# Kernel optimization log

Hardware: AMD Instinct MI355X
Metric: run time of the kernel (lower is better)

## Reference

```python
import jax, jax.numpy as jnp
import numpy as np

N_LAYER, N_HEAD, D_MODEL, D_FF = 6, 16, 1024, 4096
D_HEAD = D_MODEL // N_HEAD            # 64
M_FEAT = 2 * D_MODEL // N_HEAD        # 128, favor_feature_dims default
CHUNK = 128                           # chunk size for causal linear attention
LN_EPS = 1e-5
ATT_EPS = 1e-6                        # fast-transformers CausalLinearAttention eps
B, S = 4, 2048


def _layer_norm(x, g, b):
    mu = x.mean(-1, keepdims=True)
    var = ((x - mu) ** 2).mean(-1, keepdims=True)
    return (x - mu) * jax.lax.rsqrt(var + LN_EPS) * g + b


def _favor_phi(x, omega):
    # x: [B,H,S,Dh]; omega: [Dh, M//2]. FAVOR positive (hyperbolic) random
    # features: phi(x) = [exp(u - |x|^2/2), exp(-u - |x|^2/2)] / sqrt(M),
    # with x pre-scaled by sqrt(softmax_temp), softmax_temp = 1/sqrt(Dh).
    x = x * (D_HEAD ** -0.25)
    u = jnp.einsum('bhsd,dm->bhsm', x, omega)
    nrm = 0.5 * jnp.sum(x * x, axis=-1, keepdims=True)
    phi = jnp.concatenate([jnp.exp(u - nrm), jnp.exp(-u - nrm)], axis=-1)
    return phi * (M_FEAT ** -0.5)


def _causal_linear_attention(Qp, Kp, V):
    # Qp,Kp: [B,H,S,M] nonnegative features; V: [B,H,S,Dh].
    # out_i = phi(q_i)^T S_i / (phi(q_i)^T Z_i + eps),
    # S_i = sum_{j<=i} phi(k_j) v_j^T, Z_i = sum_{j<=i} phi(k_j).
    # Chunked: exclusive chunk prefix sums + masked intra-chunk matmul.
    b, h, s, m = Qp.shape
    d = V.shape[-1]
    c = s // CHUNK
    Qc = Qp.reshape(b, h, c, CHUNK, m)
    Kc = Kp.reshape(b, h, c, CHUNK, m)
    Vc = V.reshape(b, h, c, CHUNK, d)
    kv = jnp.einsum('bhclm,bhcld->bhcmd', Kc, Vc)   # per-chunk K^T V
    ksum = Kc.sum(axis=3)                            # [b,h,c,m]
    kv_pre = jnp.cumsum(kv, axis=2) - kv             # exclusive prefix over chunks
    ks_pre = jnp.cumsum(ksum, axis=2) - ksum
    scores = jnp.einsum('bhcim,bhcjm->bhcij', Qc, Kc)
    mask = jnp.tril(jnp.ones((CHUNK, CHUNK), bool))
    scores = jnp.where(mask, scores, 0.0)            # causal within chunk
    num = (jnp.einsum('bhcij,bhcjd->bhcid', scores, Vc)
           + jnp.einsum('bhcim,bhcmd->bhcid', Qc, kv_pre))
    den = scores.sum(-1) + jnp.einsum('bhcim,bhcm->bhci', Qc, ks_pre)
    out = num / (den[..., None] + ATT_EPS)
    return out.reshape(b, h, s, d)


def _forward(x, Wq, bq, Wk, bk, Wv, bv, Wo, bo, omega,
             g1, be1, W1, bf1, W2, bf2, g2, be2):
    bsz, slen, _ = x.shape
    out = x
    for l in range(N_LAYER):
        def proj(W, bvec):
            y = jnp.einsum('bsd,de->bse', out, W) + bvec
            return y.reshape(bsz, slen, N_HEAD, D_HEAD).transpose(0, 2, 1, 3)
        q = proj(Wq[l], bq[l])
        k = proj(Wk[l], bk[l])
        v = proj(Wv[l], bv[l])
        Qp = _favor_phi(q, omega[l])
        Kp = _favor_phi(k, omega[l])
        a = _causal_linear_attention(Qp, Kp, v)
        a = a.transpose(0, 2, 1, 3).reshape(bsz, slen, D_MODEL)
        a = jnp.einsum('bsd,de->bse', a, Wo[l]) + bo[l]
        h1 = _layer_norm(out + a, g1[l], be1[l])          # post-norm residual 1
        y = jax.nn.relu(jnp.einsum('bsd,df->bsf', h1, W1[l]) + bf1[l])
        y = jnp.einsum('bsf,fd->bsd', y, W2[l]) + bf2[l]
        out = _layer_norm(h1 + y, g2[l], be2[l])          # post-norm residual 2
    return out


def setup_inputs() -> dict:
    key = jax.random.key(0)
    ks = jax.random.split(key, 12)
    s = D_MODEL ** -0.5
    f32 = jnp.float32
    return {
        "x": jax.random.normal(ks[0], (B, S, D_MODEL), f32),
        "Wq": jax.random.normal(ks[1], (N_LAYER, D_MODEL, D_MODEL), f32) * s,
        "bq": jnp.zeros((N_LAYER, D_MODEL), f32),
        "Wk": jax.random.normal(ks[2], (N_LAYER, D_MODEL, D_MODEL), f32) * s,
        "bk": jnp.zeros((N_LAYER, D_MODEL), f32),
        "Wv": jax.random.normal(ks[3], (N_LAYER, D_MODEL, D_MODEL), f32) * s,
        "bv": jnp.zeros((N_LAYER, D_MODEL), f32),
        "Wo": jax.random.normal(ks[4], (N_LAYER, D_MODEL, D_MODEL), f32) * s,
        "bo": jnp.zeros((N_LAYER, D_MODEL), f32),
        "omega": jax.random.normal(ks[5], (N_LAYER, D_HEAD, M_FEAT // 2), f32),
        "g1": jnp.ones((N_LAYER, D_MODEL), f32),
        "be1": jnp.zeros((N_LAYER, D_MODEL), f32),
        "W1": jax.random.normal(ks[6], (N_LAYER, D_MODEL, D_FF), f32) * s,
        "bf1": jnp.zeros((N_LAYER, D_FF), f32),
        "W2": jax.random.normal(ks[7], (N_LAYER, D_FF, D_MODEL), f32) * (D_FF ** -0.5),
        "bf2": jnp.zeros((N_LAYER, D_MODEL), f32),
        "g2": jnp.ones((N_LAYER, D_MODEL), f32),
        "be2": jnp.zeros((N_LAYER, D_MODEL), f32),
    }


def reference(x, Wq, bq, Wk, bk, Wv, bv, Wo, bo, omega,
              g1, be1, W1, bf1, W2, bf2, g2, be2):
    return _forward(x, Wq, bq, Wk, bk, Wv, bv, Wo, bo, omega,
                    g1, be1, W1, bf1, W2, bf2, g2, be2)
```

## Files before the change

### kernel.cpp

```cpp
#include <hip/hip_runtime.h>

typedef unsigned short u16;
typedef __attribute__((ext_vector_type(8))) short bf16x8;
typedef __attribute__((ext_vector_type(4))) float f32x4;

#define DEV __device__ __forceinline__

DEV float b2f(u16 h){ return __uint_as_float(((unsigned)h) << 16); }
DEV u16 f2b(float f){ unsigned u = __float_as_uint(f); u += 0x7FFFu + ((u >> 16) & 1u); return (u16)(u >> 16); }

DEV void gload16(const u16* g, u16* l){
  __builtin_amdgcn_global_load_lds((const __attribute__((address_space(1))) unsigned*)g,
                                   (__attribute__((address_space(3))) unsigned*)l, 16, 0, 0);
}

__global__ __launch_bounds__(256) void wtrans(const float* __restrict__ src, u16* __restrict__ dst,
                                              int K, int N, float scale){
  __shared__ float tile[32][33];
  int k0 = blockIdx.x * 32, n0 = blockIdx.y * 32;
  int tid = threadIdx.x;
#pragma unroll
  for (int i = 0; i < 4; i++){
    int idx = tid + i * 256;
    int r = idx >> 5, c = idx & 31;
    tile[r][c] = src[(size_t)(k0 + r) * N + n0 + c];
  }
  __syncthreads();
#pragma unroll
  for (int i = 0; i < 4; i++){
    int idx = tid + i * 256;
    int r = idx >> 5, c = idx & 31;
    dst[(size_t)(n0 + r) * K + k0 + c] = f2b(tile[c][r] * scale);
  }
}

__global__ __launch_bounds__(256) void cvt16(const float* __restrict__ src, u16* __restrict__ dst){
  size_t i = ((size_t)blockIdx.x * 256 + threadIdx.x) * 4;
  float4 f = *(const float4*)(src + i);
  ushort4 o = make_ushort4(f2b(f.x), f2b(f.y), f2b(f.z), f2b(f.w));
  *(ushort4*)(dst + i) = o;
}

__global__ void catbias(const float* __restrict__ bq, const float* __restrict__ bk,
                        const float* __restrict__ bv, float* __restrict__ bcat){
  int i = blockIdx.x * 256 + threadIdx.x;
  if (i >= 6 * 3072) return;
  int l = i / 3072, j = i % 3072;
  float v = (j < 1024) ? bq[l * 1024 + j] : (j < 2048) ? bk[l * 1024 + j - 1024] : bv[l * 1024 + j - 2048];
  bcat[i] = v;
}

__global__ void fillv(float* __restrict__ p, float v, int n){
  int i = blockIdx.x * 256 + threadIdx.x;
  if (i < n) p[i] = v;
}

DEV int swz(int r){ return (r & 3) ^ ((r >> 2) & 3); }

template<int EPI>
__global__ __launch_bounds__(256) void gemm_bt(const u16* __restrict__ A, const u16* __restrict__ Bt,
                                               const float* __restrict__ bias, void* __restrict__ outp,
                                               int M, int N, int K, int ldA, int ldB){
  __shared__ __align__(16) u16 As[2][4096];
  __shared__ __align__(16) u16 Bs[2][4096];
  const int tid = threadIdx.x;
  const int lane = tid & 63;
  const int w = tid >> 6;
  const int wm = w >> 1, wn = w & 1;
  int nx = gridDim.x;
  int nwg = nx * gridDim.y;
  int lin = blockIdx.y * nx + blockIdx.x;
  int cpx = nwg >> 3;
  int sw = (lin & 7) * cpx + (lin >> 3);
  const int m0 = (sw / nx) * 128;
  const int n0 = (sw % nx) * 128;

  int r0 = tid >> 2, c0 = tid & 3;
  int r1 = r0 + 64;
  int cs0 = c0 ^ swz(r0);
  int cs1 = c0 ^ swz(r1);
  const u16* ag0 = A + (size_t)(m0 + r0) * ldA + cs0 * 8;
  const u16* ag1 = A + (size_t)(m0 + r1) * ldA + cs1 * 8;
  const u16* bg0 = Bt + (size_t)(n0 + r0) * ldB + cs0 * 8;
  const u16* bg1 = Bt + (size_t)(n0 + r1) * ldB + cs1 * 8;

  f32x4 acc[4][4] = {};
  const int KT = K >> 5;

  gload16(ag0, &As[0][w * 512]);
  gload16(ag1, &As[0][2048 + w * 512]);
  gload16(bg0, &Bs[0][w * 512]);
  gload16(bg1, &Bs[0][2048 + w * 512]);

  for (int kt = 0; kt < KT; kt++){
    int cur = kt & 1;
    if (kt + 1 < KT){
      int ko = (kt + 1) << 5;
      gload16(ag0 + ko, &As[cur ^ 1][w * 512]);
      gload16(ag1 + ko, &As[cur ^ 1][2048 + w * 512]);
      gload16(bg0 + ko, &Bs[cur ^ 1][w * 512]);
      gload16(bg1 + ko, &Bs[cur ^ 1][2048 + w * 512]);
      asm volatile("s_waitcnt vmcnt(4)" ::: "memory");
    } else {
      asm volatile("s_waitcnt vmcnt(0)" ::: "memory");
    }
    __builtin_amdgcn_s_barrier();
    bf16x8 fa[4], fb[4];
#pragma unroll
    for (int m = 0; m < 4; m++){
      int row = wm * 64 + m * 16 + (lane & 15);
      int cc = (lane >> 4) ^ swz(row);
      fa[m] = *(const bf16x8*)(&As[cur][row * 32 + cc * 8]);
    }
#pragma unroll
    for (int n = 0; n < 4; n++){
      int row = wn * 64 + n * 16 + (lane & 15);
      int cc = (lane >> 4) ^ swz(row);
      fb[n] = *(const bf16x8*)(&Bs[cur][row * 32 + cc * 8]);
    }
#pragma unroll
    for (int m = 0; m < 4; m++)
#pragma unroll
      for (int n = 0; n < 4; n++)
        acc[m][n] = __builtin_amdgcn_mfma_f32_16x16x32_bf16(fa[m], fb[n], acc[m][n], 0, 0, 0);
    asm volatile("s_waitcnt lgkmcnt(0)" ::: "memory");
    __builtin_amdgcn_s_barrier();
  }

#pragma unroll
  for (int m = 0; m < 4; m++){
    int rowb = m0 + wm * 64 + m * 16 + ((lane >> 4) << 2);
#pragma unroll
    for (int n = 0; n < 4; n++){
      int col = n0 + wn * 64 + n * 16 + (lane & 15);
      float bv = bias[col];
      if (EPI == 5 && col >= 2048){
        int cv = col - 2048, hh = cv >> 6, dh = cv & 63;
        int bIdx = rowb >> 11, s4 = rowb & 2047;
        ushort4 pk = make_ushort4(f2b(acc[m][n][0] + bv), f2b(acc[m][n][1] + bv),
                                  f2b(acc[m][n][2] + bv), f2b(acc[m][n][3] + bv));
        *(ushort4*)&((u16*)outp + 16777216)[((size_t)(bIdx * 16 + hh) * 64 + dh) * 2048 + s4] = pk;
      } else {
#pragma unroll
        for (int r = 0; r < 4; r++){
          float v = acc[m][n][r] + bv;
          int rr = rowb + r;
          if (EPI == 5){
            u16* dst0 = (u16*)outp + (col < 1024 ? 0 : 8388608);
            int cv = col & 1023, hh = cv >> 6, dh = cv & 63;
            int bIdx = rr >> 11, s = rr & 2047;
            dst0[(((size_t)(bIdx * 16 + hh) * 2048 + s) << 6) + dh] = f2b(v);
          } else if (EPI == 2){
            ((u16*)outp)[(size_t)rr * N + col] = f2b(v > 0.f ? v : 0.f);
          } else {
            ((u16*)outp)[(size_t)rr * N + col] = f2b(v);
          }
        }
      }
    }
  }
}

template<int EPI>
__global__ __launch_bounds__(512, 1) void gemm8p(const u16* __restrict__ A, const u16* __restrict__ Bt,
                                                 const float* __restrict__ bias, void* __restrict__ outp,
                                                 int M, int N, int K, int ldA, int ldB){
  __shared__ __align__(16) u16 As[2][16384];
  __shared__ __align__(16) u16 Bs[2][16384];
  const int tid = threadIdx.x;
  const int lane = tid & 63;
  const int w = tid >> 6;
  const int wm = w >> 2, wn = w & 3;
  int nx = gridDim.x;
  int nwg = nx * gridDim.y;
  int lin = blockIdx.y * nx + blockIdx.x;
  int cpx = nwg >> 3;
  int sw = (lin & 7) * cpx + (lin >> 3);
  const int m0 = (sw / nx) * 256;
  const int n0 = (sw % nx) * 256;

  const int id1 = 512 + tid;
  const int r0 = tid >> 2, c20 = tid & 3;
  const int r1 = id1 >> 2, c21 = id1 & 3;
  const int cs0 = c20 ^ ((r0 >> 1) & 3);
  const int cs1 = c21 ^ ((r1 >> 1) & 3);
  const u16* Ag0 = A + (size_t)(m0 + r0) * ldA + cs0 * 8;
  const u16* Ag1 = A + (size_t)(m0 + r1) * ldA + cs1 * 8;
  const u16* Bg0 = Bt + (size_t)(n0 + r0) * ldB + cs0 * 8;
  const u16* Bg1 = Bt + (size_t)(n0 + r1) * ldB + cs1 * 8;

  f32x4 acc[8][4] = {};
  const int KT = K >> 6;

  auto stA = [&](int buf, int kt, int ks){
    int kc = kt * 64 + ks * 32;
    gload16(Ag0 + kc, &As[buf][ks * 8192 + w * 512]);
    gload16(Ag1 + kc, &As[buf][ks * 8192 + 4096 + w * 512]);
  };
  auto stB = [&](int buf, int kt, int ks){
    int kc = kt * 64 + ks * 32;
    gload16(Bg0 + kc, &Bs[buf][ks * 8192 + w * 512]);
    gload16(Bg1 + kc, &Bs[buf][ks * 8192 + 4096 + w * 512]);
  };

  stA(0, 0, 0); stB(0, 0, 0); stA(0, 0, 1); stB(0, 0, 1);

  for (int t = 0; t < KT; t++){
    int c = t & 1, nb = c ^ 1;
    bool pf = (t + 1 < KT);
    asm volatile("s_waitcnt vmcnt(4)" ::: "memory");
    __builtin_amdgcn_s_barrier();

#pragma unroll
    for (int ks = 0; ks < 2; ks++){
      if (ks == 1){
        if (pf) asm volatile("s_waitcnt vmcnt(4)" ::: "memory");
        else    asm volatile("s_waitcnt vmcnt(0)" ::: "memory");
        __builtin_amdgcn_s_barrier();
      }
      if (pf){ if (ks == 0) stA(nb, t + 1, 0); else stA(nb, t + 1, 1); }
      bf16x8 fa[8], fb[2];
#pragma unroll
      for (int m = 0; m < 8; m++){
        int row = wm * 128 + m * 16 + (lane & 15);
        int slot = (lane >> 4) ^ ((row >> 1) & 3);
        fa[m] = *(const bf16x8*)(&As[c][ks * 8192 + row * 32 + slot * 8]);
      }
#pragma unroll
      for (int nn = 0; nn < 2; nn++){
        int row = wn * 64 + nn * 16 + (lane & 15);
        int slot = (lane >> 4) ^ ((row >> 1) & 3);
        fb[nn] = *(const bf16x8*)(&Bs[c][ks * 8192 + row * 32 + slot * 8]);
      }
      __builtin_amdgcn_s_setprio(1);
#pragma unroll
      for (int m = 0; m < 8; m++)
#pragma unroll
        for (int nn = 0; nn < 2; nn++)
          acc[m][nn] = __builtin_amdgcn_mfma_f32_16x16x32_bf16(fa[m], fb[nn], acc[m][nn], 0, 0, 0);
      __builtin_amdgcn_s_setprio(0);
      if (pf){ if (ks == 0) stB(nb, t + 1, 0); else stB(nb, t + 1, 1); }
#pragma unroll
      for (int nn = 0; nn < 2; nn++){
        int row = wn * 64 + 32 + nn * 16 + (lane & 15);
        int slot = (lane >> 4) ^ ((row >> 1) & 3);
        fb[nn] = *(const bf16x8*)(&Bs[c][ks * 8192 + row * 32 + slot * 8]);
      }
      __builtin_amdgcn_s_setprio(1);
#pragma unroll
      for (int m = 0; m < 8; m++)
#pragma unroll
        for (int nn = 0; nn < 2; nn++)
          acc[m][2 + nn] = __builtin_amdgcn_mfma_f32_16x16x32_bf16(fa[m], fb[nn], acc[m][2 + nn], 0, 0, 0);
      __builtin_amdgcn_s_setprio(0);
    }
  }

#pragma unroll
  for (int m = 0; m < 8; m++){
    int rowb = m0 + wm * 128 + m * 16 + ((lane >> 4) << 2);
#pragma unroll
    for (int n = 0; n < 4; n++){
      int col = n0 + wn * 64 + n * 16 + (lane & 15);
      float bv = bias[col];
#pragma unroll
      for (int r = 0; r < 4; r++){
        float v = acc[m][n][r] + bv;
        int rr = rowb + r;
        if (EPI == 2) ((u16*)outp)[(size_t)rr * N + col] = f2b(v > 0.f ? v : 0.f);
        else          ((u16*)outp)[(size_t)rr * N + col] = f2b(v);
      }
    }
  }
}

__global__ __launch_bounds__(512, 1) void gemm8pk(const u16* __restrict__ A, const u16* __restrict__ Bt,
                                                  const float* __restrict__ bias0, const float* __restrict__ bias1,
                                                  u16* __restrict__ out0, u16* __restrict__ out1,
                                                  int M, int N, int Khalf, int ldA, int ldB){
  __shared__ __align__(16) u16 As[2][16384];
  __shared__ __align__(16) u16 Bs[2][16384];
  const int tid = threadIdx.x;
  const int lane = tid & 63;
  const int w = tid >> 6;
  const int wm = w >> 2, wn = w & 3;
  int lin = blockIdx.x;
  int cpx = gridDim.x >> 3;
  int sw = (lin & 7) * cpx + (lin >> 3);
  const int kz = sw & 1;
  const int t2 = sw >> 1;
  const int n0 = (t2 & 3) * 256;
  const int m0 = (t2 >> 2) * 256;
  const u16* Ab = A + kz * Khalf;
  const u16* Bb = Bt + kz * Khalf;
  u16* outp = kz ? out1 : out0;
  const float* bias = kz ? bias1 : bias0;

  const int id1 = 512 + tid;
  const int r0 = tid >> 2, c20 = tid & 3;
  const int r1 = id1 >> 2, c21 = id1 & 3;
  const int cs0 = c20 ^ ((r0 >> 1) & 3);
  const int cs1 = c21 ^ ((r1 >> 1) & 3);
  const u16* Ag0 = Ab + (size_t)(m0 + r0) * ldA + cs0 * 8;
  const u16* Ag1 = Ab + (size_t)(m0 + r1) * ldA + cs1 * 8;
  const u16* Bg0 = Bb + (size_t)(n0 + r0) * ldB + cs0 * 8;
  const u16* Bg1 = Bb + (size_t)(n0 + r1) * ldB + cs1 * 8;

  f32x4 acc[8][4] = {};
  const int KT = Khalf >> 6;

  auto stA = [&](int buf, int kt, int ks){
    int kc = kt * 64 + ks * 32;
    gload16(Ag0 + kc, &As[buf][ks * 8192 + w * 512]);
    gload16(Ag1 + kc, &As[buf][ks * 8192 + 4096 + w * 512]);
  };
  auto stB = [&](int buf, int kt, int ks){
    int kc = kt * 64 + ks * 32;
    gload16(Bg0 + kc, &Bs[buf][ks * 8192 + w * 512]);
    gload16(Bg1 + kc, &Bs[buf][ks * 8192 + 4096 + w * 512]);
  };

  stA(0, 0, 0); stB(0, 0, 0); stA(0, 0, 1); stB(0, 0, 1);

  for (int t = 0; t < KT; t++){
    int c = t & 1, nb = c ^ 1;
    bool pf = (t + 1 < KT);
    asm volatile("s_waitcnt vmcnt(4)" ::: "memory");
    __builtin_amdgcn_s_barrier();

#pragma unroll
    for (int ks = 0; ks < 2; ks++){
      if (ks == 1){
        if (pf) asm volatile("s_waitcnt vmcnt(4)" ::: "memory");
        else    asm volatile("s_waitcnt vmcnt(0)" ::: "memory");
        __builtin_amdgcn_s_barrier();
      }
      if (pf){ if (ks == 0) stA(nb, t + 1, 0); else stA(nb, t + 1, 1); }
      bf16x8 fa[8], fb[2];
#pragma unroll
      for (int m = 0; m < 8; m++){
        int row = wm * 128 + m * 16 + (lane & 15);
        int slot = (lane >> 4) ^ ((row >> 1) & 3);
        fa[m] = *(const bf16x8*)(&As[c][ks * 8192 + row * 32 + slot * 8]);
      }
#pragma unroll
      for (int nn = 0; nn < 2; nn++){
        int row = wn * 64 + nn * 16 + (lane & 15);
        int slot = (lane >> 4) ^ ((row >> 1) & 3);
        fb[nn] = *(const bf16x8*)(&Bs[c][ks * 8192 + row * 32 + slot * 8]);
      }
      __builtin_amdgcn_s_setprio(1);
#pragma unroll
      for (int m = 0; m < 8; m++)
#pragma unroll
        for (int nn = 0; nn < 2; nn++)
          acc[m][nn] = __builtin_amdgcn_mfma_f32_16x16x32_bf16(fa[m], fb[nn], acc[m][nn], 0, 0, 0);
      __builtin_amdgcn_s_setprio(0);
      if (pf){ if (ks == 0) stB(nb, t + 1, 0); else stB(nb, t + 1, 1); }
#pragma unroll
      for (int nn = 0; nn < 2; nn++){
        int row = wn * 64 + 32 + nn * 16 + (lane & 15);
        int slot = (lane >> 4) ^ ((row >> 1) & 3);
        fb[nn] = *(const bf16x8*)(&Bs[c][ks * 8192 + row * 32 + slot * 8]);
      }
      __builtin_amdgcn_s_setprio(1);
#pragma unroll
      for (int m = 0; m < 8; m++)
#pragma unroll
        for (int nn = 0; nn < 2; nn++)
          acc[m][2 + nn] = __builtin_amdgcn_mfma_f32_16x16x32_bf16(fa[m], fb[nn], acc[m][2 + nn], 0, 0, 0);
      __builtin_amdgcn_s_setprio(0);
    }
  }

#pragma unroll
  for (int m = 0; m < 8; m++){
    int rowb = m0 + wm * 128 + m * 16 + ((lane >> 4) << 2);
#pragma unroll
    for (int n = 0; n < 4; n++){
      int col = n0 + wn * 64 + n * 16 + (lane & 15);
      float bv = bias[col];
#pragma unroll
      for (int r = 0; r < 4; r++)
        outp[(size_t)(rowb + r) * N + col] = f2b(acc[m][n][r] + bv);
    }
  }
}

__global__ __launch_bounds__(256) void phi2(const u16* __restrict__ qb, const u16* __restrict__ kb,
                                            const u16* __restrict__ omT,
                                            u16* __restrict__ Qp, u16* __restrict__ Kp){
  __shared__ __align__(16) u16 qs[128 * 64];
  __shared__ __align__(16) u16 wl[64 * 64];
  __shared__ __align__(16) u16 ph[128 * 128];
  __shared__ float part[2][128];
  __shared__ float nrm[128];
  int tid = threadIdx.x, w = tid >> 6, lane = tid & 63;
  int blk = blockIdx.x;
  const u16* src; u16* dst; int row0;
  if (blk < 1024){ src = qb; dst = Qp; row0 = blk * 128; }
  else           { src = kb; dst = Kp; row0 = (blk - 1024) * 128; }
  const u16* g = src + (size_t)row0 * 64;
#pragma unroll
  for (int i = 0; i < 4; i++){
    int id = tid * 4 + i;
    int r = id >> 3, kc = id & 7;
    *(bf16x8*)(qs + r * 64 + ((kc ^ (r & 7)) << 3)) = *(const bf16x8*)(g + r * 64 + kc * 8);
  }
#pragma unroll
  for (int i = 0; i < 2; i++){
    int id = tid * 2 + i;
    int m = id >> 3, kc = id & 7;
    *(bf16x8*)(wl + m * 64 + ((kc ^ (m & 7)) << 3)) = *(const bf16x8*)(omT + id * 8);
  }
  __syncthreads();
  {
    int r = tid & 127, half = tid >> 7;
    float s = 0.f;
#pragma unroll
    for (int j = 0; j < 4; j++){
      int kc = half * 4 + j;
      bf16x8 v = *(const bf16x8*)(qs + r * 64 + ((kc ^ (r & 7)) << 3));
#pragma unroll
      for (int e = 0; e < 8; e++){ float f = b2f((u16)v[e]); s += f * f; }
    }
    part[half][r] = s;
  }
  __syncthreads();
  if (tid < 128) nrm[tid] = 0.0625f * (part[0][tid] + part[1][tid]);
  __syncthreads();
  f32x4 acc[2][4] = {};
#pragma unroll
  for (int kt = 0; kt < 2; kt++){
    int kc = kt * 4 + (lane >> 4);
    bf16x8 fa[2], fb[4];
#pragma unroll
    for (int mt = 0; mt < 2; mt++){
      int r = w * 32 + mt * 16 + (lane & 15);
      fa[mt] = *(const bf16x8*)(qs + r * 64 + ((kc ^ (r & 7)) << 3));
    }
#pragma unroll
    for (int nt = 0; nt < 4; nt++){
      int m = nt * 16 + (lane & 15);
      fb[nt] = *(const bf16x8*)(wl + m * 64 + ((kc ^ (m & 7)) << 3));
    }
#pragma unroll
    for (int mt = 0; mt < 2; mt++)
#pragma unroll
      for (int nt = 0; nt < 4; nt++)
        acc[mt][nt] = __builtin_amdgcn_mfma_f32_16x16x32_bf16(fa[mt], fb[nt], acc[mt][nt], 0, 0, 0);
  }
  const float LNC = -2.4260151319598086f;
#pragma unroll
  for (int mt = 0; mt < 2; mt++)
#pragma unroll
    for (int nt = 0; nt < 4; nt++)
#pragma unroll
      for (int r4 = 0; r4 < 4; r4++){
        int r = w * 32 + mt * 16 + ((lane >> 4) << 2) + r4;
        int m = nt * 16 + (lane & 15);
        float u = acc[mt][nt][r4];
        float nr = nrm[r];
        ph[r * 128 + m]      = f2b(__expf(u - nr + LNC));
        ph[r * 128 + 64 + m] = f2b(__expf(-u - nr + LNC));
      }
  __syncthreads();
  u16* go = dst + (size_t)row0 * 128;
#pragma unroll
  for (int i = 0; i < 8; i++){
    int id = i * 256 + tid;
    *(bf16x8*)(go + id * 8) = *(const bf16x8*)(ph + id * 8);
  }
}

__global__ __launch_bounds__(256) void kvchunk(const u16* __restrict__ Kp, const u16* __restrict__ vt,
                                               float* __restrict__ kv, float* __restrict__ ksum){
  __shared__ __align__(16) u16 Ks[128 * 128];
  __shared__ __align__(16) u16 Vst[64 * 128];
  int blk = blockIdx.x; int bh = blk >> 4, c = blk & 15;
  int tid = threadIdx.x;
  size_t base = (size_t)bh * 2048 + c * 128;
  const u16* Kc = Kp + base * 128;
  const u16* vtc = vt + (size_t)bh * 64 * 2048 + c * 128;
  {
    int j = tid >> 1, half = tid & 1;
#pragma unroll
    for (int i = 0; i < 8; i++)
      *(bf16x8*)(Ks + j * 128 + half * 64 + i * 8) = *(const bf16x8*)(Kc + j * 128 + half * 64 + i * 8);
#pragma unroll
    for (int i = 0; i < 4; i++){
      int id = tid * 4 + i;
      int d = id >> 4, mc = id & 15;
      *(bf16x8*)(Vst + d * 128 + mc * 8) = *(const bf16x8*)(vtc + (size_t)d * 2048 + mc * 8);
    }
  }
  __syncthreads();
  int tm = tid & 15, td = tid >> 4;
  int mbase = tm * 8, dbase = td * 4;
  float acc[8][4] = {};
  float ks[8] = {};
  for (int i = 0; i < 128; i++){
    bf16x8 kk = *(const bf16x8*)(Ks + i * 128 + mbase);
    float kf[8];
#pragma unroll
    for (int e = 0; e < 8; e++) kf[e] = b2f((u16)kk[e]);
    float vf[4];
#pragma unroll
    for (int e = 0; e < 4; e++) vf[e] = b2f(Vst[(dbase + e) * 128 + i]);
#pragma unroll
    for (int a = 0; a < 8; a++){
      ks[a] += kf[a];
#pragma unroll
      for (int bb = 0; bb < 4; bb++) acc[a][bb] += kf[a] * vf[bb];
    }
  }
  float* kvout = kv + ((size_t)bh * 16 + c) * 8192;
#pragma unroll
  for (int a = 0; a < 8; a++)
#pragma unroll
    for (int bb = 0; bb < 4; bb++)
      kvout[(size_t)(dbase + bb) * 128 + mbase + a] = acc[a][bb];
  if (td == 0){
    float* kso = ksum + ((size_t)bh * 16 + c) * 128;
#pragma unroll
    for (int a = 0; a < 8; a++) kso[mbase + a] = ks[a];
  }
}

__global__ __launch_bounds__(256) void kvscan(float* __restrict__ kv, float* __restrict__ ksum){
  int bh = blockIdx.x;
  int p = blockIdx.y;
  int tid = threadIdx.x;
  if (p < 8){
    size_t base = (size_t)bh * 16 * 8192;
    int idx0 = p * 1024 + tid;
    for (int rep = 0; rep < 4; rep++){
      int idx = idx0 + rep * 256;
      float run = 0.f;
#pragma unroll
      for (int c = 0; c < 16; c++){
        size_t off = base + (size_t)c * 8192 + idx;
        float v = kv[off]; kv[off] = run; run += v;
      }
    }
  } else if (tid < 128){
    size_t base = (size_t)bh * 16 * 128;
    float run = 0.f;
#pragma unroll
    for (int c = 0; c < 16; c++){
      size_t off = base + c * 128 + tid;
      float v = ksum[off]; ksum[off] = run; run += v;
    }
  }
}

__global__ __launch_bounds__(512) void attn_fused(const u16* __restrict__ Qp, const u16* __restrict__ Kp,
                                                  const u16* __restrict__ vt, const float* __restrict__ kvp,
                                                  const float* __restrict__ ksum, u16* __restrict__ aout){
  __shared__ __align__(16) u16 sm[53248];
  int blk = blockIdx.x, bh = blk >> 4, c = blk & 15;
  int b = bh >> 4, h = bh & 15;
  int tid = threadIdx.x, w = tid >> 6, lane = tid & 63;
  size_t base = (size_t)bh * 2048 + c * 128;
  const u16* Qc = Qp + base * 128;
  const u16* Kc = Kp + base * 128;
  const u16* vtc = vt + (size_t)bh * 64 * 2048 + c * 128;
  const float* kvc = kvp + ((size_t)bh * 16 + c) * 8192;
  const float* ksc = ksum + ((size_t)bh * 16 + c) * 128;
  u16* Qs = sm;
  u16* Ks = sm + 16384;
  u16* B2 = sm + 32768;

#pragma unroll
  for (int i = 0; i < 4; i++){
    int id = tid * 4 + i;
    int r = id >> 4, kc = id & 15;
    int swo = (kc ^ (r & 15)) << 3;
    *(bf16x8*)(Qs + r * 128 + swo) = *(const bf16x8*)(Qc + (size_t)r * 128 + kc * 8);
    *(bf16x8*)(Ks + r * 128 + swo) = *(const bf16x8*)(Kc + (size_t)r * 128 + kc * 8);
  }
#pragma unroll
  for (int i = 0; i < 2; i++){
    int id = tid * 2 + i;
    int d = id >> 4, kc = id & 15;
    *(bf16x8*)(B2 + d * 256 + ((kc ^ (d & 31)) << 3)) = *(const bf16x8*)(vtc + (size_t)d * 2048 + kc * 8);
  }
#pragma unroll
  for (int i = 0; i < 2; i++){
    int id = tid * 2 + i;
    int d = id >> 4, mc = id & 15;
    const float* s8 = kvc + d * 128 + mc * 8;
    float4 f0 = *(const float4*)(s8);
    float4 f1 = *(const float4*)(s8 + 4);
    bf16x8 pk;
    pk[0] = (short)f2b(f0.x); pk[1] = (short)f2b(f0.y); pk[2] = (short)f2b(f0.z); pk[3] = (short)f2b(f0.w);
    pk[4] = (short)f2b(f1.x); pk[5] = (short)f2b(f1.y); pk[6] = (short)f2b(f1.z); pk[7] = (short)f2b(f1.w);
    int kc = 16 + mc;
    *(bf16x8*)(B2 + d * 256 + ((kc ^ (d & 31)) << 3)) = pk;
  }
  {
    int row = 64 + (tid >> 5), kc = tid & 31;
    bf16x8 pk = {};
    if (row == 64){
      if (kc < 16){
#pragma unroll
        for (int e = 0; e < 8; e++) pk[e] = (short)0x3F80;
      } else {
        const float* s8 = ksc + (kc - 16) * 8;
        float4 f0 = *(const float4*)(s8);
        float4 f1 = *(const float4*)(s8 + 4);
        pk[0] = (short)f2b(f0.x); pk[1] = (short)f2b(f0.y); pk[2] = (short)f2b(f0.z); pk[3] = (short)f2b(f0.w);
        pk[4] = (short)f2b(f1.x); pk[5] = (short)f2b(f1.y); pk[6] = (short)f2b(f1.z); pk[7] = (short)f2b(f1.w);
      }
    }
    *(bf16x8*)(B2 + row * 256 + ((kc ^ (row & 31)) << 3)) = pk;
  }
  __syncthreads();

  int wm = w >> 2, wn = w & 3;
  f32x4 acc1[4][2] = {};
#pragma unroll
  for (int kk = 0; kk < 4; kk++){
    int kc = kk * 4 + (lane >> 4);
    bf16x8 fa[4], fb[2];
#pragma unroll
    for (int m = 0; m < 4; m++){
      int row = wm * 64 + m * 16 + (lane & 15);
      fa[m] = *(const bf16x8*)(Qs + row * 128 + ((kc ^ (row & 15)) << 3));
    }
#pragma unroll
    for (int n = 0; n < 2; n++){
      int row = wn * 32 + n * 16 + (lane & 15);
      fb[n] = *(const bf16x8*)(Ks + row * 128 + ((kc ^ (row & 15)) << 3));
    }
#pragma unroll
    for (int m = 0; m < 4; m++)
#pragma unroll
      for (int n = 0; n < 2; n++)
        acc1[m][n] = __builtin_amdgcn_mfma_f32_16x16x32_bf16(fa[m], fb[n], acc1[m][n], 0, 0, 0);
  }
  __syncthreads();

#pragma unroll
  for (int m = 0; m < 4; m++)
#pragma unroll
    for (int n = 0; n < 2; n++)
#pragma unroll
      for (int r = 0; r < 4; r++){
        int i = wm * 64 + m * 16 + ((lane >> 4) << 2) + r;
        int j = wn * 32 + n * 16 + (lane & 15);
        float v = (j <= i) ? acc1[m][n][r] : 0.f;
        Ks[i * 128 + (((j >> 3) ^ (i & 15)) << 3) + (j & 7)] = f2b(v);
      }
  __syncthreads();

  f32x4 acc2[5] = {};
#pragma unroll
  for (int kk = 0; kk < 8; kk++){
    int kc = kk * 4 + (lane >> 4);
    int rowA = w * 16 + (lane & 15);
    bf16x8 fa2;
    if (kk < 4) fa2 = *(const bf16x8*)(Ks + rowA * 128 + ((kc ^ (rowA & 15)) << 3));
    else        fa2 = *(const bf16x8*)(Qs + rowA * 128 + (((kc - 16) ^ (rowA & 15)) << 3));
#pragma unroll
    for (int n = 0; n < 5; n++){
      int d = n * 16 + (lane & 15);
      bf16x8 fb2 = *(const bf16x8*)(B2 + d * 256 + ((kc ^ (d & 31)) << 3));
      acc2[n] = __builtin_amdgcn_mfma_f32_16x16x32_bf16(fa2, fb2, acc2[n], 0, 0, 0);
    }
  }

  float dd[4];
#pragma unroll
  for (int r = 0; r < 4; r++) dd[r] = __shfl(acc2[4][r], lane & 48) + 1e-6f;
  size_t obase = ((size_t)b * 2048 + c * 128) * 1024 + (size_t)h * 64;
#pragma unroll
  for (int n = 0; n < 4; n++)
#pragma unroll
    for (int r = 0; r < 4; r++){
      int i = w * 16 + ((lane >> 4) << 2) + r;
      int d = n * 16 + (lane & 15);
      aout[obase + (size_t)i * 1024 + d] = f2b(acc2[n][r] / dd[r]);
    }
}

__global__ __launch_bounds__(256) void ln_kernel(const float* __restrict__ X1, const u16* __restrict__ X2b,
                                                 const float* __restrict__ g, const float* __restrict__ bb,
                                                 float* __restrict__ outf, u16* __restrict__ outb){
  __shared__ float red[2][4];
  int row = blockIdx.x, tid = threadIdx.x, w = tid >> 6, lane = tid & 63;
  size_t ro = (size_t)row * 1024 + tid * 4;
  float4 a = *(const float4*)(X1 + ro);
  ushort4 bp = *(const ushort4*)(X2b + ro);
  float x0 = a.x + b2f(bp.x), x1 = a.y + b2f(bp.y), x2 = a.z + b2f(bp.z), x3 = a.w + b2f(bp.w);
  float s1 = x0 + x1 + x2 + x3;
  float s2 = x0 * x0 + x1 * x1 + x2 * x2 + x3 * x3;
#pragma unroll
  for (int off = 32; off; off >>= 1){ s1 += __shfl_xor(s1, off); s2 += __shfl_xor(s2, off); }
  if (lane == 0){ red[0][w] = s1; red[1][w] = s2; }
  __syncthreads();
  float t1 = red[0][0] + red[0][1] + red[0][2] + red[0][3];
  float t2 = red[1][0] + red[1][1] + red[1][2] + red[1][3];
  float mu = t1 * (1.f / 1024.f);
  float var = t2 * (1.f / 1024.f) - mu * mu;
  float rs = rsqrtf(var + 1e-5f);
  float4 gv = *(const float4*)(g + tid * 4);
  float4 bv = *(const float4*)(bb + tid * 4);
  float o0 = (x0 - mu) * rs * gv.x + bv.x;
  float o1 = (x1 - mu) * rs * gv.y + bv.y;
  float o2 = (x2 - mu) * rs * gv.z + bv.z;
  float o3 = (x3 - mu) * rs * gv.w + bv.w;
  *(float4*)(outf + ro) = make_float4(o0, o1, o2, o3);
  *(ushort4*)(outb + ro) = make_ushort4(f2b(o0), f2b(o1), f2b(o2), f2b(o3));
}

__global__ __launch_bounds__(256) void ln3_kernel(const float* __restrict__ X1, const u16* __restrict__ P0,
                                                  const u16* P1, const float* __restrict__ g,
                                                  const float* __restrict__ bb,
                                                  float* __restrict__ outf, u16* outb){
  __shared__ float red[2][4];
  int row = blockIdx.x, tid = threadIdx.x, w = tid >> 6, lane = tid & 63;
  size_t ro = (size_t)row * 1024 + tid * 4;
  float4 a = *(const float4*)(X1 + ro);
  ushort4 p0 = *(const ushort4*)(P0 + ro);
  ushort4 p1 = *(const ushort4*)(P1 + ro);
  float x0 = a.x + b2f(p0.x) + b2f(p1.x);
  float x1 = a.y + b2f(p0.y) + b2f(p1.y);
  float x2 = a.z + b2f(p0.z) + b2f(p1.z);
  float x3 = a.w + b2f(p0.w) + b2f(p1.w);
  float s1 = x0 + x1 + x2 + x3;
  float s2 = x0 * x0 + x1 * x1 + x2 * x2 + x3 * x3;
#pragma unroll
  for (int off = 32; off; off >>= 1){ s1 += __shfl_xor(s1, off); s2 += __shfl_xor(s2, off); }
  if (lane == 0){ red[0][w] = s1; red[1][w] = s2; }
  __syncthreads();
  float t1 = red[0][0] + red[0][1] + red[0][2] + red[0][3];
  float t2 = red[1][0] + red[1][1] + red[1][2] + red[1][3];
  float mu = t1 * (1.f / 1024.f);
  float var = t2 * (1.f / 1024.f) - mu * mu;
  float rs = rsqrtf(var + 1e-5f);
  float4 gv = *(const float4*)(g + tid * 4);
  float4 bv = *(const float4*)(bb + tid * 4);
  float o0 = (x0 - mu) * rs * gv.x + bv.x;
  float o1 = (x1 - mu) * rs * gv.y + bv.y;
  float o2 = (x2 - mu) * rs * gv.z + bv.z;
  float o3 = (x3 - mu) * rs * gv.w + bv.w;
  *(float4*)(outf + ro) = make_float4(o0, o1, o2, o3);
  *(ushort4*)(outb + ro) = make_ushort4(f2b(o0), f2b(o1), f2b(o2), f2b(o3));
}

extern "C" void kernel_launch(void* const* d_in, const int* in_sizes, int n_in,
                              void* d_out, int out_size, void* d_ws, size_t ws_size,
                              hipStream_t stream){
  (void)in_sizes; (void)n_in;
  const float* x   = (const float*)d_in[0];
  const float* Wq  = (const float*)d_in[1];
  const float* bq  = (const float*)d_in[2];
  const float* Wk  = (const float*)d_in[3];
  const float* bk  = (const float*)d_in[4];
  const float* Wv  = (const float*)d_in[5];
  const float* bv  = (const float*)d_in[6];
  const float* Wo  = (const float*)d_in[7];
  const float* bo  = (const float*)d_in[8];
  const float* om  = (const float*)d_in[9];
  const float* g1  = (const float*)d_in[10];
  const float* be1 = (const float*)d_in[11];
  const float* W1  = (const float*)d_in[12];
  const float* bf1 = (const float*)d_in[13];
  const float* W2  = (const float*)d_in[14];
  const float* bf2 = (const float*)d_in[15];
  const float* g2  = (const float*)d_in[16];
  const float* be2 = (const float*)d_in[17];

  char* ws = (char*)d_ws;
  size_t off = 0;
  auto alloc = [&](size_t bytes) -> void* {
    void* p = ws + off; off += (bytes + 255) & ~(size_t)255; return p;
  };
  u16* Wcat = (u16*)alloc(3072ull * 1024 * 2);
  u16* Wot  = (u16*)alloc(1024ull * 1024 * 2);
  u16* W1t  = (u16*)alloc(4096ull * 1024 * 2);
  u16* W2t  = (u16*)alloc(1024ull * 4096 * 2);
  u16* omT  = (u16*)alloc(64ull * 64 * 2);
  float* bcat = (float*)alloc(6ull * 3072 * 4);
  float* zbuf = (float*)alloc(1024 * 4);
  u16* Xb  = (u16*)alloc(8192ull * 1024 * 2);
  u16* qb  = (u16*)alloc(131072ull * 64 * 2);
  u16* kb  = (u16*)alloc(131072ull * 64 * 2);
  u16* vt  = (u16*)alloc(131072ull * 64 * 2);
  u16* Qp  = (u16*)alloc(131072ull * 128 * 2);
  u16* Kp  = (u16*)alloc(131072ull * 128 * 2);
  float* ksum = (float*)alloc(64ull * 16 * 128 * 4);

  if (off > ws_size){
    fillv<<<(out_size + 255) / 256, 256, 0, stream>>>((float*)d_out, (float)(ws_size >> 20), out_size);
    return;
  }

  float* kvbuf  = (float*)qb;
  u16*  ybuf   = qb;
  u16*  wooutb = Qp;
  u16*  w2outb = Qp + 8388608;
  float* h1     = (float*)Kp;
  float* resid  = (float*)d_out;

  cvt16<<<8192, 256, 0, stream>>>(x, Xb);
  catbias<<<72, 256, 0, stream>>>(bq, bk, bv, bcat);
  fillv<<<4, 256, 0, stream>>>(zbuf, 0.f, 1024);

  const float* Xsrc = x;
  for (int l = 0; l < 6; l++){
    size_t o1k = (size_t)l * 1024 * 1024;
    size_t o4k = (size_t)l * 4096 * 1024;
    wtrans<<<dim3(32, 32), 256, 0, stream>>>(Wq + o1k, Wcat, 1024, 1024, 1.f);
    wtrans<<<dim3(32, 32), 256, 0, stream>>>(Wk + o1k, Wcat + 1024ull * 1024, 1024, 1024, 1.f);
    wtrans<<<dim3(32, 32), 256, 0, stream>>>(Wv + o1k, Wcat + 2048ull * 1024, 1024, 1024, 1.f);
    wtrans<<<dim3(32, 32), 256, 0, stream>>>(Wo + o1k, Wot, 1024, 1024, 1.f);
    wtrans<<<dim3(32, 128), 256, 0, stream>>>(W1 + o4k, W1t, 1024, 4096, 1.f);
    wtrans<<<dim3(128, 32), 256, 0, stream>>>(W2 + o4k, W2t, 4096, 1024, 1.f);
    wtrans<<<dim3(2, 2), 256, 0, stream>>>(om + (size_t)l * 4096, omT, 64, 64, 0.35355339059327373f);

    gemm_bt<5><<<dim3(24, 64), 256, 0, stream>>>(Xb, Wcat, bcat + l * 3072, qb, 8192, 3072, 1024, 1024, 1024);
    phi2<<<2048, 256, 0, stream>>>(qb, kb, omT, Qp, Kp);
    kvchunk<<<1024, 256, 0, stream>>>(Kp, vt, kvbuf, ksum);
    kvscan<<<dim3(64, 9), 256, 0, stream>>>(kvbuf, ksum);
    attn_fused<<<1024, 512, 0, stream>>>(Qp, Kp, vt, kvbuf, ksum, Xb);
    gemm_bt<6><<<dim3(8, 64), 256, 0, stream>>>(Xb, Wot, bo + l * 1024, wooutb, 8192, 1024, 1024, 1024, 1024);
    ln_kernel<<<8192, 256, 0, stream>>>(Xsrc, wooutb, g1 + l * 1024, be1 + l * 1024, h1, Xb);
    gemm8p<2><<<dim3(16, 32), 512, 0, stream>>>(Xb, W1t, bf1 + l * 4096, ybuf, 8192, 4096, 1024, 1024, 1024);
    gemm8pk<<<dim3(256), 512, 0, stream>>>(ybuf, W2t, bf2 + l * 1024, zbuf, w2outb, Xb,
                                           8192, 1024, 2048, 4096, 4096);
    ln3_kernel<<<8192, 256, 0, stream>>>(h1, w2outb, Xb, g2 + l * 1024, be2 + l * 1024, resid, Xb);
    Xsrc = resid;
  }
}
```

Measured before the change: 2.579 ms.

## Batch weight transposes across layers and stage ReLU GEMM epilogue through LDS

Weight conversion/transposition for all six layers is now done up front in seven batched launches (grid z over layers) into per-layer buffers, instead of seven small launches per layer, when workspace allows; otherwise it falls back to per-layer transposes. Separately, the ReLU epilogue of gemm8p now writes the bf16 tile into shared memory with an XOR swizzle and then stores coalesced 16-byte rows to global, replacing scattered 2-byte stores. This cuts launch count and improves store coalescing at the cost of more workspace and an extra LDS round trip with two barriers.

```diff
diff --git a/kernel.cpp b/kernel.cpp
--- a/kernel.cpp
+++ b/kernel.cpp
@@ -17,6 +17,28 @@
 __global__ __launch_bounds__(256) void wtrans(const float* __restrict__ src, u16* __restrict__ dst,
                                               int K, int N, float scale){
   __shared__ float tile[32][33];
+  int k0 = blockIdx.x * 32, n0 = blockIdx.y * 32;
+  int tid = threadIdx.x;
+#pragma unroll
+  for (int i = 0; i < 4; i++){
+    int idx = tid + i * 256;
+    int r = idx >> 5, c = idx & 31;
+    tile[r][c] = src[(size_t)(k0 + r) * N + n0 + c];
+  }
+  __syncthreads();
+#pragma unroll
+  for (int i = 0; i < 4; i++){
+    int idx = tid + i * 256;
+    int r = idx >> 5, c = idx & 31;
+    dst[(size_t)(n0 + r) * K + k0 + c] = f2b(tile[c][r] * scale);
+  }
+}
+
+__global__ __launch_bounds__(256) void wtransb(const float* __restrict__ src0, u16* __restrict__ dst0,
+                                               int K, int N, float scale, size_t sstride, size_t dstride){
+  __shared__ float tile[32][33];
+  const float* src = src0 + blockIdx.z * sstride;
+  u16* dst = dst0 + blockIdx.z * dstride;
   int k0 = blockIdx.x * 32, n0 = blockIdx.y * 32;
   int tid = threadIdx.x;
 #pragma unroll
@@ -256,6 +278,39 @@
     }
   }
 
+  if (EPI == 2){
+    __syncthreads();
+    u16* Cl = wm ? (u16*)&Bs[0][0] : (u16*)&As[0][0];
+#pragma unroll
+    for (int m = 0; m < 8; m++){
+#pragma unroll
+      for (int n = 0; n < 4; n++){
+        int col = wn * 64 + n * 16 + (lane & 15);
+        float bv = bias[n0 + col];
+#pragma unroll
+        for (int r = 0; r < 4; r++){
+          int row = m * 16 + ((lane >> 4) << 2) + r;
+          int X = ((row >> 2) & 3) << 4;
+          float v = acc[m][n][r] + bv;
+          Cl[row * 256 + (col ^ X)] = f2b(v > 0.f ? v : 0.f);
+        }
+      }
+    }
+    __syncthreads();
+#pragma unroll
+    for (int i = 0; i < 16; i++){
+      int id = i * 512 + tid;
+      int half = id >> 12;
+      int idx = id & 4095;
+      int row_l = idx >> 5, ck = idx & 31;
+      int X = ((row_l >> 2) & 3) << 4;
+      const u16* srcp = (half ? (const u16*)&Bs[0][0] : (const u16*)&As[0][0]) + row_l * 256 + ((ck * 8) ^ X);
+      u16* gdst = (u16*)outp + (size_t)(m0 + half * 128 + row_l) * N + n0 + ck * 8;
+      *(bf16x8*)gdst = *(const bf16x8*)srcp;
+    }
+    return;
+  }
+
 #pragma unroll
   for (int m = 0; m < 8; m++){
     int rowb = m0 + wm * 128 + m * 16 + ((lane >> 4) << 2);
@@ -267,8 +322,7 @@
       for (int r = 0; r < 4; r++){
         float v = acc[m][n][r] + bv;
         int rr = rowb + r;
-        if (EPI == 2) ((u16*)outp)[(size_t)rr * N + col] = f2b(v > 0.f ? v : 0.f);
-        else          ((u16*)outp)[(size_t)rr * N + col] = f2b(v);
+        ((u16*)outp)[(size_t)rr * N + col] = f2b(v);
       }
     }
   }
@@ -777,11 +831,6 @@
   auto alloc = [&](size_t bytes) -> void* {
     void* p = ws + off; off += (bytes + 255) & ~(size_t)255; return p;
   };
-  u16* Wcat = (u16*)alloc(3072ull * 1024 * 2);
-  u16* Wot  = (u16*)alloc(1024ull * 1024 * 2);
-  u16* W1t  = (u16*)alloc(4096ull * 1024 * 2);
-  u16* W2t  = (u16*)alloc(1024ull * 4096 * 2);
-  u16* omT  = (u16*)alloc(64ull * 64 * 2);
   float* bcat = (float*)alloc(6ull * 3072 * 4);
   float* zbuf = (float*)alloc(1024 * 4);
   u16* Xb  = (u16*)alloc(8192ull * 1024 * 2);
@@ -791,7 +840,22 @@
   u16* Qp  = (u16*)alloc(131072ull * 128 * 2);
   u16* Kp  = (u16*)alloc(131072ull * 128 * 2);
   float* ksum = (float*)alloc(64ull * 16 * 128 * 4);
-
+  size_t base_end = off;
+
+  u16* Wcat6 = (u16*)alloc(6ull * 3072 * 1024 * 2);
+  u16* Wot6  = (u16*)alloc(6ull * 1024 * 1024 * 2);
+  u16* W1t6  = (u16*)alloc(6ull * 4096 * 1024 * 2);
+  u16* W2t6  = (u16*)alloc(6ull * 4096 * 1024 * 2);
+  u16* omT6  = (u16*)alloc(6ull * 64 * 64 * 2);
+  bool hoist = (off <= ws_size);
+  if (!hoist){
+    off = base_end;
+    Wcat6 = (u16*)alloc(3072ull * 1024 * 2);
+    Wot6  = (u16*)alloc(1024ull * 1024 * 2);
+    W1t6  = (u16*)alloc(4096ull * 1024 * 2);
+    W2t6  = (u16*)alloc(4096ull * 1024 * 2);
+    omT6  = (u16*)alloc(64ull * 64 * 2);
+  }
   if (off > ws_size){
     fillv<<<(out_size + 255) / 256, 256, 0, stream>>>((float*)d_out, (float)(ws_size >> 20), out_size);
     return;
@@ -808,27 +872,44 @@
   catbias<<<72, 256, 0, stream>>>(bq, bk, bv, bcat);
   fillv<<<4, 256, 0, stream>>>(zbuf, 0.f, 1024);
 
+  if (hoist){
+    wtransb<<<dim3(32, 32, 6), 256, 0, stream>>>(Wq, Wcat6, 1024, 1024, 1.f, 1048576, 3145728);
+    wtransb<<<dim3(32, 32, 6), 256, 0, stream>>>(Wk, Wcat6 + 1048576, 1024, 1024, 1.f, 1048576, 3145728);
+    wtransb<<<dim3(32, 32, 6), 256, 0, stream>>>(Wv, Wcat6 + 2097152, 1024, 1024, 1.f, 1048576, 3145728);
+    wtransb<<<dim3(32, 32, 6), 256, 0, stream>>>(Wo, Wot6, 1024, 1024, 1.f, 1048576, 1048576);
+    wtransb<<<dim3(32, 128, 6), 256, 0, stream>>>(W1, W1t6, 1024, 4096, 1.f, 4194304, 4194304);
+    wtransb<<<dim3(128, 32, 6), 256, 0, stream>>>(W2, W2t6, 4096, 1024, 1.f, 4194304, 4194304);
+    wtransb<<<dim3(2, 2, 6), 256, 0, stream>>>(om, omT6, 64, 64, 0.35355339059327373f, 4096, 4096);
+  }
+
   const float* Xsrc = x;
   for (int l = 0; l < 6; l++){
     size_t o1k = (size_t)l * 1024 * 1024;
     size_t o4k = (size_t)l * 4096 * 1024;
-    wtrans<<<dim3(32, 32), 256, 0, stream>>>(Wq + o1k, Wcat, 1024, 1024, 1.f);
-    wtrans<<<dim3(32, 32), 256, 0, stream>>>(Wk + o1k, Wcat + 1024ull * 1024, 1024, 1024, 1.f);
-    wtrans<<<dim3(32, 32), 256, 0, stream>>>(Wv + o1k, Wcat + 2048ull * 1024, 1024, 1024, 1.f);
-    wtrans<<<dim3(32, 32), 256, 0, stream>>>(Wo + o1k, Wot, 1024, 1024, 1.f);
-    wtrans<<<dim3(32, 128), 256, 0, stream>>>(W1 + o4k, W1t, 1024, 4096, 1.f);
-    wtrans<<<dim3(128, 32), 256, 0, stream>>>(W2 + o4k, W2t, 4096, 1024, 1.f);
-    wtrans<<<dim3(2, 2), 256, 0, stream>>>(om + (size_t)l * 4096, omT, 64, 64, 0.35355339059327373f);
-
-    gemm_bt<5><<<dim3(24, 64), 256, 0, stream>>>(Xb, Wcat, bcat + l * 3072, qb, 8192, 3072, 1024, 1024, 1024);
-    phi2<<<2048, 256, 0, stream>>>(qb, kb, omT, Qp, Kp);
+    const u16* wcat = Wcat6 + (hoist ? (size_t)l * 3072 * 1024 : 0);
+    const u16* wot  = Wot6  + (hoist ? o1k : 0);
+    const u16* w1t  = W1t6  + (hoist ? o4k : 0);
+    const u16* w2t  = W2t6  + (hoist ? o4k : 0);
+    const u16* omTl = omT6  + (hoist ? (size_t)l * 4096 : 0);
+    if (!hoist){
+      wtrans<<<dim3(32, 32), 256, 0, stream>>>(Wq + o1k, Wcat6, 1024, 1024, 1.f);
+      wtrans<<<dim3(32, 32), 256, 0, stream>>>(Wk + o1k, Wcat6 + 1048576, 1024, 1024, 1.f);
+      wtrans<<<dim3(32, 32), 256, 0, stream>>>(Wv + o1k, Wcat6 + 2097152, 1024, 1024, 1.f);
+      wtrans<<<dim3(32, 32), 256, 0, stream>>>(Wo + o1k, Wot6, 1024, 1024, 1.f);
+      wtrans<<<dim3(32, 128), 256, 0, stream>>>(W1 + o4k, W1t6, 1024, 4096, 1.f);
+      wtrans<<<dim3(128, 32), 256, 0, stream>>>(W2 + o4k, W2t6, 4096, 1024, 1.f);
+      wtrans<<<dim3(2, 2), 256, 0, stream>>>(om + (size_t)l * 4096, omT6, 64, 64, 0.35355339059327373f);
+    }
+
+    gemm_bt<5><<<dim3(24, 64), 256, 0, stream>>>(Xb, wcat, bcat + l * 3072, qb, 8192, 3072, 1024, 1024, 1024);
+    phi2<<<2048, 256, 0, stream>>>(qb, kb, omTl, Qp, Kp);
     kvchunk<<<1024, 256, 0, stream>>>(Kp, vt, kvbuf, ksum);
     kvscan<<<dim3(64, 9), 256, 0, stream>>>(kvbuf, ksum);
     attn_fused<<<1024, 512, 0, stream>>>(Qp, Kp, vt, kvbuf, ksum, Xb);
-    gemm_bt<6><<<dim3(8, 64), 256, 0, stream>>>(Xb, Wot, bo + l * 1024, wooutb, 8192, 1024, 1024, 1024, 1024);
+    gemm_bt<6><<<dim3(8, 64), 256, 0, stream>>>(Xb, wot, bo + l * 1024, wooutb, 8192, 1024, 1024, 1024, 1024);
     ln_kernel<<<8192, 256, 0, stream>>>(Xsrc, wooutb, g1 + l * 1024, be1 + l * 1024, h1, Xb);
-    gemm8p<2><<<dim3(16, 32), 512, 0, stream>>>(Xb, W1t, bf1 + l * 4096, ybuf, 8192, 4096, 1024, 1024, 1024);
-    gemm8pk<<<dim3(256), 512, 0, stream>>>(ybuf, W2t, bf2 + l * 1024, zbuf, w2outb, Xb,
+    gemm8p<2><<<dim3(16, 32), 512, 0, stream>>>(Xb, w1t, bf1 + l * 4096, ybuf, 8192, 4096, 1024, 1024, 1024);
+    gemm8pk<<<dim3(256), 512, 0, stream>>>(ybuf, w2t, bf2 + l * 1024, zbuf, w2outb, Xb,
                                            8192, 1024, 2048, 4096, 4096);
     ln3_kernel<<<8192, 256, 0, stream>>>(h1, w2outb, Xb, g2 + l * 1024, be2 + l * 1024, resid, Xb);
     Xsrc = resid;
```

New measurement: 2.623 ms. Within noise of the previous version (+1.7%).
